# Kernel tuning notes

Hardware: AMD Instinct MI355X
Metric: run time of the kernel (lower is better)

The kernel has to match this reference:

```python
import jax, jax.numpy as jnp
import numpy as np

N_FRAMES = 100000
HIDDEN = 512
N_QUERIES = 256
N_EVENTS = 2048
TOPK = 8
FRAME_RATE = 5.0
EPS = 1e-12


def setup_inputs() -> dict:
    key = jax.random.key(0)
    k1, k2, k3, k4 = jax.random.split(key, 4)
    video_feats = jax.random.normal(k1, (1, N_FRAMES, HIDDEN), dtype=jnp.float32)
    query_feats = jax.random.normal(k2, (N_QUERIES, HIDDEN), dtype=jnp.float32)
    video_events = jnp.sort(
        jax.random.randint(k3, (N_FRAMES,), 0, N_EVENTS, dtype=jnp.int32))
    W_reg = jax.random.normal(k4, (HIDDEN, 2), dtype=jnp.float32) * 0.02
    b_reg = jnp.zeros((2,), dtype=jnp.float32)
    return {"video_feats": video_feats, "query_feats": query_feats,
            "video_events": video_events, "W_reg": W_reg, "b_reg": b_reg}


def reference(video_feats, query_feats, video_events, W_reg, b_reg):
    vf = video_feats[0]                                   # [N, D]
    n = vf.shape[0]
    # --- per-event masked-mean pooling (segment mean) ---
    sums = jax.ops.segment_sum(vf, video_events, num_segments=N_EVENTS)          # [E, D]
    counts = jax.ops.segment_sum(jnp.ones((n,), vf.dtype), video_events,
                                 num_segments=N_EVENTS)                          # [E]
    event_avg = sums / jnp.maximum(counts, 1.0)[:, None]                         # [E, D]
    # --- event timestamps: first/last frame index per event / frame_rate ---
    idx = jnp.arange(n, dtype=jnp.int32)
    start = jax.ops.segment_min(idx, video_events, num_segments=N_EVENTS)
    end = jax.ops.segment_max(idx, video_events, num_segments=N_EVENTS)
    # empty events get int extremes; zero them out (they have zero features anyway)
    nonempty = counts > 0
    start = jnp.where(nonempty, start, 0)
    end = jnp.where(nonempty, end, 0)
    event_ts = jnp.stack([start, end], axis=-1).astype(jnp.float32) / FRAME_RATE  # [E, 2]
    # --- cosine similarity query x event ---
    qn = query_feats / jnp.maximum(
        jnp.linalg.norm(query_feats, axis=-1, keepdims=True), EPS)
    en = event_avg / jnp.maximum(
        jnp.linalg.norm(event_avg, axis=-1, keepdims=True), EPS)
    sim = qn @ en.T                                       # [Q, E]
    # --- per-query top-k event selection ---
    _, top_idx = jax.lax.top_k(sim, TOPK)                 # [Q, K]
    sel_ts = event_ts[top_idx]                            # [Q, K, 2]
    sel_dur = sel_ts[..., 1] - sel_ts[..., 0]             # [Q, K]
    sel_feat = event_avg[top_idx]                         # [Q, K, D]
    interact = sel_feat * query_feats[:, None, :]         # [Q, K, D]
    bbox_bias = jnp.tanh(jnp.einsum('qkd,dt->qkt', interact, W_reg) + b_reg)  # [Q, K, 2]
    pred_timestamps = sel_ts + bbox_bias * sel_dur[..., None]
    return pred_timestamps
```

## Files before the change

### kernel.cpp

```cpp
#include <hip/hip_runtime.h>
#include <hip/hip_bf16.h>
#include <math.h>

#define N_FRAMES 100000
#define HIDDEN 512
#define N_QUERIES 256
#define N_EVENTS 2048
#define TOPK 8
#define FRAME_RATE 5.0f
#define EPSN 1e-12f


__global__ void init_k(int* __restrict__ start, int* __restrict__ end) {
    int e = blockIdx.x * blockDim.x + threadIdx.x;
    if (e < N_EVENTS) { start[e] = -1; end[e] = -1; }
}

__global__ void bounds_k(const int* __restrict__ ev, int* __restrict__ start,
                         int* __restrict__ end) {
    int i = blockIdx.x * blockDim.x + threadIdx.x;
    if (i >= N_FRAMES) return;
    int e = ev[i];
    if (i == 0 || ev[i - 1] != e) start[e] = i;
    if (i == N_FRAMES - 1 || ev[i + 1] != e) end[e] = i;
}

__global__ void pool_k(const float* __restrict__ vf, const int* __restrict__ start,
                       const int* __restrict__ end, float* __restrict__ avg,
                       float* __restrict__ inv_en, float* __restrict__ ts) {
    int e = blockIdx.x;
    int s = start[e], t = end[e];
    int tid = threadIdx.x;
    int half = tid >> 7;
    int l = tid & 127;
    float4 acc = make_float4(0.f, 0.f, 0.f, 0.f);
    if (s >= 0) {
        const float4* p = (const float4*)vf + (size_t)(s + half) * 128 + l;
        int f = s + half;
        for (; f + 2 <= t; f += 4, p += 512) {
            float4 v0 = p[0];
            float4 v1 = p[256];
            acc.x += v0.x + v1.x; acc.y += v0.y + v1.y;
            acc.z += v0.z + v1.z; acc.w += v0.w + v1.w;
        }
        if (f <= t) {
            float4 v0 = *p;
            acc.x += v0.x; acc.y += v0.y; acc.z += v0.z; acc.w += v0.w;
        }
    }
    __shared__ float4 buf[128];
    __shared__ float ssbuf[2];
    if (half) buf[l] = acc;
    __syncthreads();
    if (!half) {
        float4 o = buf[l];
        acc.x += o.x; acc.y += o.y; acc.z += o.z; acc.w += o.w;
        if (s >= 0) {
            float cnt = (float)(t - s + 1);
            acc.x = acc.x / cnt; acc.y = acc.y / cnt;
            acc.z = acc.z / cnt; acc.w = acc.w / cnt;
        }
        *((float4*)avg + (size_t)e * 128 + l) = acc;
        float ss = acc.x * acc.x + acc.y * acc.y + acc.z * acc.z + acc.w * acc.w;
        #pragma unroll
        for (int off = 32; off; off >>= 1) ss += __shfl_xor(ss, off);
        if ((tid & 63) == 0) ssbuf[tid >> 6] = ss;
    }
    __syncthreads();
    if (tid == 0) {
        float ss = ssbuf[0] + ssbuf[1];
        inv_en[e] = (s >= 0) ? 1.0f / fmaxf(sqrtf(ss), EPSN) : 0.0f;
        ts[e * 2 + 0] = (s >= 0) ? (float)s / FRAME_RATE : 0.0f;
        ts[e * 2 + 1] = (s >= 0) ? (float)t / FRAME_RATE : 0.0f;
    }
}

__global__ void qnorm_k(const float* __restrict__ qf, float* __restrict__ inv_qn) {
    int q = blockIdx.x;
    int lane = threadIdx.x;
    const float* row = qf + (size_t)q * HIDDEN;
    float ss = 0.f;
    #pragma unroll
    for (int i = 0; i < 8; ++i) { float v = row[lane + 64 * i]; ss += v * v; }
    #pragma unroll
    for (int off = 32; off; off >>= 1) ss += __shfl_xor(ss, off);
    if (lane == 0) inv_qn[q] = 1.0f / fmaxf(sqrtf(ss), EPSN);
}

#define BQ 64
#define BE 32
#define DC 128
#define DCP 132

__global__ void sim_k(const float* __restrict__ qf, const float* __restrict__ avg,
                      const float* __restrict__ inv_qn, const float* __restrict__ inv_en,
                      float* __restrict__ sim) {
    __shared__ float qs[BQ][DCP];
    __shared__ float es[BE][DCP];
    int tid = threadIdx.x;
    int qbase = blockIdx.y * BQ;
    int ebase = blockIdx.x * BE;
    int e0 = tid & 15;
    int q0 = tid >> 4;
    float acc[4][2] = {{0.f, 0.f}, {0.f, 0.f}, {0.f, 0.f}, {0.f, 0.f}};
    for (int dc = 0; dc < HIDDEN; dc += DC) {
        __syncthreads();
        #pragma unroll
        for (int r = 0; r < 8; ++r) {
            int ldx = tid + 256 * r;
            int row = ldx >> 5, c4 = ldx & 31;
            float4 v = *(const float4*)(qf + (size_t)(qbase + row) * HIDDEN + dc + c4 * 4);
            *(float4*)&qs[row][c4 * 4] = v;
        }
        #pragma unroll
        for (int r = 0; r < 4; ++r) {
            int ldx = tid + 256 * r;
            int row = ldx >> 5, c4 = ldx & 31;
            float4 v = *(const float4*)(avg + (size_t)(ebase + row) * HIDDEN + dc + c4 * 4);
            *(float4*)&es[row][c4 * 4] = v;
        }
        __syncthreads();
        #pragma unroll 4
        for (int d = 0; d < DC; d += 4) {
            float4 ev0 = *(const float4*)&es[e0][d];
            float4 ev1 = *(const float4*)&es[e0 + 16][d];
            #pragma unroll
            for (int i = 0; i < 4; ++i) {
                float4 qv = *(const float4*)&qs[q0 + 16 * i][d];
                acc[i][0] += qv.x * ev0.x + qv.y * ev0.y + qv.z * ev0.z + qv.w * ev0.w;
                acc[i][1] += qv.x * ev1.x + qv.y * ev1.y + qv.z * ev1.z + qv.w * ev1.w;
            }
        }
    }
    float iq[4];
    #pragma unroll
    for (int i = 0; i < 4; ++i) iq[i] = inv_qn[qbase + q0 + 16 * i];
    float ie0 = inv_en[ebase + e0];
    float ie1 = inv_en[ebase + e0 + 16];
    #pragma unroll
    for (int i = 0; i < 4; ++i) {
        size_t rowoff = (size_t)(qbase + q0 + 16 * i) * N_EVENTS + ebase;
        sim[rowoff + e0] = acc[i][0] * iq[i] * ie0;
        sim[rowoff + e0 + 16] = acc[i][1] * iq[i] * ie1;
    }
}

__global__ void topk_k(const float* __restrict__ sim, int* __restrict__ top_idx) {
    int q = blockIdx.x;
    int lane = threadIdx.x;
    const float* row = sim + (size_t)q * N_EVENTS;
    float v[32];
    #pragma unroll
    for (int i = 0; i < 32; ++i) v[i] = row[lane + 64 * i];
    int chosen[TOPK];
    #pragma unroll
    for (int k = 0; k < TOPK; ++k) {
        float best = -INFINITY;
        int bidx = 0x7fffffff;
        #pragma unroll
        for (int i = 0; i < 32; ++i) {
            int idx = lane + 64 * i;
            bool dup = false;
            #pragma unroll
            for (int j = 0; j < TOPK; ++j) dup = dup || ((j < k) && (chosen[j] == idx));
            if (!dup && v[i] > best) { best = v[i]; bidx = idx; }
        }
        #pragma unroll
        for (int off = 32; off; off >>= 1) {
            float ov = __shfl_xor(best, off);
            int oi = __shfl_xor(bidx, off);
            if (ov > best || (ov == best && oi < bidx)) { best = ov; bidx = oi; }
        }
        chosen[k] = bidx;
        if (lane == 0) top_idx[q * TOPK + k] = bidx;
    }
}

__global__ void final_k(const float* __restrict__ avg, const float* __restrict__ qf,
                        const float* __restrict__ ts, const int* __restrict__ top_idx,
                        const float* __restrict__ W, const float* __restrict__ b,
                        float* __restrict__ out) {
    int blk = blockIdx.x;
    int q = blk >> 3;
    int lane = threadIdx.x;
    int e = top_idx[blk];
    const float* frow = avg + (size_t)e * HIDDEN;
    const float* qrow = qf + (size_t)q * HIDDEN;
    float a0 = 0.f, a1 = 0.f;
    #pragma unroll
    for (int i = 0; i < 8; ++i) {
        int d = lane + 64 * i;
        float f = frow[d] * qrow[d];
        a0 += f * W[d * 2 + 0];
        a1 += f * W[d * 2 + 1];
    }
    #pragma unroll
    for (int off = 32; off; off >>= 1) {
        a0 += __shfl_xor(a0, off);
        a1 += __shfl_xor(a1, off);
    }
    if (lane == 0) {
        float b0 = tanhf(a0 + b[0]);
        float b1 = tanhf(a1 + b[1]);
        float t0 = ts[e * 2 + 0], t1 = ts[e * 2 + 1];
        float dur = t1 - t0;
        out[blk * 2 + 0] = t0 + b0 * dur;
        out[blk * 2 + 1] = t1 + b1 * dur;
    }
}

extern "C" void kernel_launch(void* const* d_in, const int* in_sizes, int n_in,
                              void* d_out, int out_size, void* d_ws, size_t ws_size,
                              hipStream_t stream) {
    const float* vf = (const float*)d_in[0];
    const float* qf = (const float*)d_in[1];
    const int* ev = (const int*)d_in[2];
    const float* W = (const float*)d_in[3];
    const float* b = (const float*)d_in[4];
    float* out = (float*)d_out;

    char* ws = (char*)d_ws;
    float* avg    = (float*)(ws + 0);
    float* ts     = (float*)(ws + 4194304);
    float* inv_en = (float*)(ws + 4210688);
    float* inv_qn = (float*)(ws + 4218880);
    int*   start  = (int*)  (ws + 4219904);
    int*   endp   = (int*)  (ws + 4228096);
    float* sim    = (float*)(ws + 4236288);
    int*   tidx   = (int*)  (ws + 6333440);

    init_k<<<(N_EVENTS + 255) / 256, 256, 0, stream>>>(start, endp);
    bounds_k<<<(N_FRAMES + 255) / 256, 256, 0, stream>>>(ev, start, endp);
    pool_k<<<N_EVENTS, 256, 0, stream>>>(vf, start, endp, avg, inv_en, ts);
    qnorm_k<<<N_QUERIES, 64, 0, stream>>>(qf, inv_qn);
    dim3 sgrid(N_EVENTS / BE, N_QUERIES / BQ);
    sim_k<<<sgrid, 256, 0, stream>>>(qf, avg, inv_qn, inv_en, sim);
    topk_k<<<N_QUERIES, 64, 0, stream>>>(sim, tidx);
    final_k<<<N_QUERIES * TOPK, 64, 0, stream>>>(avg, qf, ts, tidx, W, b, out);
}
```

Baseline: 335.0 us.

## Fuse init with query norm, merge topk with regressor, enlarge sim tiles

Merges the event-bounds init and the query-norm kernels into one launch, and fuses top-k selection with the bbox regressor so the top indices stay in registers and each query's weights and features are loaded once. The similarity kernel moves to 128 threads, each computing a 4x4 output tile instead of 4x2. Top-k now reads the sim row as float4. The net effect is two fewer launches and less global traffic, at the cost of lower parallelism in the final stage and in sim_k.

New measurement: 352.4 us. +5.2%, slower.

```diff
diff --git a/kernel.cpp b/kernel.cpp
--- a/kernel.cpp
+++ b/kernel.cpp
@@ -11,9 +11,22 @@
 #define EPSN 1e-12f
 
 
-__global__ void init_k(int* __restrict__ start, int* __restrict__ end) {
-    int e = blockIdx.x * blockDim.x + threadIdx.x;
-    if (e < N_EVENTS) { start[e] = -1; end[e] = -1; }
+__global__ void initq_k(const float* __restrict__ qf, float* __restrict__ inv_qn,
+                        int* __restrict__ start, int* __restrict__ end) {
+    int blk = blockIdx.x;
+    int lane = threadIdx.x;
+    if (blk < N_QUERIES) {
+        const float* row = qf + (size_t)blk * HIDDEN;
+        float ss = 0.f;
+        #pragma unroll
+        for (int i = 0; i < 8; ++i) { float v = row[lane + 64 * i]; ss += v * v; }
+        #pragma unroll
+        for (int off = 32; off; off >>= 1) ss += __shfl_xor(ss, off);
+        if (lane == 0) inv_qn[blk] = 1.0f / fmaxf(sqrtf(ss), EPSN);
+    } else {
+        int e = (blk - N_QUERIES) * 64 + lane;
+        start[e] = -1; end[e] = -1;
+    }
 }
 
 __global__ void bounds_k(const int* __restrict__ ev, int* __restrict__ start,
@@ -57,8 +70,7 @@
         acc.x += o.x; acc.y += o.y; acc.z += o.z; acc.w += o.w;
         if (s >= 0) {
             float cnt = (float)(t - s + 1);
-            acc.x = acc.x / cnt; acc.y = acc.y / cnt;
-            acc.z = acc.z / cnt; acc.w = acc.w / cnt;
+            acc.x /= cnt; acc.y /= cnt; acc.z /= cnt; acc.w /= cnt;
         }
         *((float4*)avg + (size_t)e * 128 + l) = acc;
         float ss = acc.x * acc.x + acc.y * acc.y + acc.z * acc.z + acc.w * acc.w;
@@ -73,18 +85,6 @@
         ts[e * 2 + 0] = (s >= 0) ? (float)s / FRAME_RATE : 0.0f;
         ts[e * 2 + 1] = (s >= 0) ? (float)t / FRAME_RATE : 0.0f;
     }
-}
-
-__global__ void qnorm_k(const float* __restrict__ qf, float* __restrict__ inv_qn) {
-    int q = blockIdx.x;
-    int lane = threadIdx.x;
-    const float* row = qf + (size_t)q * HIDDEN;
-    float ss = 0.f;
-    #pragma unroll
-    for (int i = 0; i < 8; ++i) { float v = row[lane + 64 * i]; ss += v * v; }
-    #pragma unroll
-    for (int off = 32; off; off >>= 1) ss += __shfl_xor(ss, off);
-    if (lane == 0) inv_qn[q] = 1.0f / fmaxf(sqrtf(ss), EPSN);
 }
 
 #define BQ 64
@@ -100,70 +100,85 @@
     int tid = threadIdx.x;
     int qbase = blockIdx.y * BQ;
     int ebase = blockIdx.x * BE;
-    int e0 = tid & 15;
-    int q0 = tid >> 4;
-    float acc[4][2] = {{0.f, 0.f}, {0.f, 0.f}, {0.f, 0.f}, {0.f, 0.f}};
+    int q0 = tid >> 3;
+    int e0 = tid & 7;
+    float acc[4][4] = {{0.f,0.f,0.f,0.f},{0.f,0.f,0.f,0.f},
+                       {0.f,0.f,0.f,0.f},{0.f,0.f,0.f,0.f}};
     for (int dc = 0; dc < HIDDEN; dc += DC) {
         __syncthreads();
         #pragma unroll
+        for (int r = 0; r < 16; ++r) {
+            int ldx = tid + 128 * r;
+            int row = ldx >> 5, c4 = ldx & 31;
+            *(float4*)&qs[row][c4 * 4] =
+                *(const float4*)(qf + (size_t)(qbase + row) * HIDDEN + dc + c4 * 4);
+        }
+        #pragma unroll
         for (int r = 0; r < 8; ++r) {
-            int ldx = tid + 256 * r;
+            int ldx = tid + 128 * r;
             int row = ldx >> 5, c4 = ldx & 31;
-            float4 v = *(const float4*)(qf + (size_t)(qbase + row) * HIDDEN + dc + c4 * 4);
-            *(float4*)&qs[row][c4 * 4] = v;
-        }
-        #pragma unroll
-        for (int r = 0; r < 4; ++r) {
-            int ldx = tid + 256 * r;
-            int row = ldx >> 5, c4 = ldx & 31;
-            float4 v = *(const float4*)(avg + (size_t)(ebase + row) * HIDDEN + dc + c4 * 4);
-            *(float4*)&es[row][c4 * 4] = v;
+            *(float4*)&es[row][c4 * 4] =
+                *(const float4*)(avg + (size_t)(ebase + row) * HIDDEN + dc + c4 * 4);
         }
         __syncthreads();
-        #pragma unroll 4
+        #pragma unroll 2
         for (int d = 0; d < DC; d += 4) {
             float4 ev0 = *(const float4*)&es[e0][d];
-            float4 ev1 = *(const float4*)&es[e0 + 16][d];
+            float4 ev1 = *(const float4*)&es[e0 + 8][d];
+            float4 ev2 = *(const float4*)&es[e0 + 16][d];
+            float4 ev3 = *(const float4*)&es[e0 + 24][d];
             #pragma unroll
             for (int i = 0; i < 4; ++i) {
                 float4 qv = *(const float4*)&qs[q0 + 16 * i][d];
                 acc[i][0] += qv.x * ev0.x + qv.y * ev0.y + qv.z * ev0.z + qv.w * ev0.w;
                 acc[i][1] += qv.x * ev1.x + qv.y * ev1.y + qv.z * ev1.z + qv.w * ev1.w;
+                acc[i][2] += qv.x * ev2.x + qv.y * ev2.y + qv.z * ev2.z + qv.w * ev2.w;
+                acc[i][3] += qv.x * ev3.x + qv.y * ev3.y + qv.z * ev3.z + qv.w * ev3.w;
             }
         }
     }
-    float iq[4];
+    float iq[4], ie[4];
     #pragma unroll
     for (int i = 0; i < 4; ++i) iq[i] = inv_qn[qbase + q0 + 16 * i];
-    float ie0 = inv_en[ebase + e0];
-    float ie1 = inv_en[ebase + e0 + 16];
+    #pragma unroll
+    for (int j = 0; j < 4; ++j) ie[j] = inv_en[ebase + e0 + 8 * j];
     #pragma unroll
     for (int i = 0; i < 4; ++i) {
         size_t rowoff = (size_t)(qbase + q0 + 16 * i) * N_EVENTS + ebase;
-        sim[rowoff + e0] = acc[i][0] * iq[i] * ie0;
-        sim[rowoff + e0 + 16] = acc[i][1] * iq[i] * ie1;
-    }
-}
-
-__global__ void topk_k(const float* __restrict__ sim, int* __restrict__ top_idx) {
+        #pragma unroll
+        for (int j = 0; j < 4; ++j)
+            sim[rowoff + e0 + 8 * j] = acc[i][j] * iq[i] * ie[j];
+    }
+}
+
+__global__ void topk_final_k(const float* __restrict__ sim, const float* __restrict__ ts,
+                             const float* __restrict__ avg, const float* __restrict__ qf,
+                             const float* __restrict__ W, const float* __restrict__ b,
+                             float* __restrict__ out) {
     int q = blockIdx.x;
     int lane = threadIdx.x;
-    const float* row = sim + (size_t)q * N_EVENTS;
-    float v[32];
-    #pragma unroll
-    for (int i = 0; i < 32; ++i) v[i] = row[lane + 64 * i];
+    const float4* row4 = (const float4*)(sim + (size_t)q * N_EVENTS);
+    float4 v4[8];
+    #pragma unroll
+    for (int g = 0; g < 8; ++g) v4[g] = row4[lane + 64 * g];
     int chosen[TOPK];
     #pragma unroll
     for (int k = 0; k < TOPK; ++k) {
         float best = -INFINITY;
         int bidx = 0x7fffffff;
         #pragma unroll
-        for (int i = 0; i < 32; ++i) {
-            int idx = lane + 64 * i;
-            bool dup = false;
+        for (int g = 0; g < 8; ++g) {
             #pragma unroll
-            for (int j = 0; j < TOPK; ++j) dup = dup || ((j < k) && (chosen[j] == idx));
-            if (!dup && v[i] > best) { best = v[i]; bidx = idx; }
+            for (int j = 0; j < 4; ++j) {
+                int idx = 4 * lane + 256 * g + j;
+                float val = (j == 0) ? v4[g].x : (j == 1) ? v4[g].y
+                          : (j == 2) ? v4[g].z : v4[g].w;
+                bool dup = false;
+                #pragma unroll
+                for (int m = 0; m < TOPK; ++m)
+                    dup = dup || ((m < k) && (chosen[m] == idx));
+                if (!dup && val > best) { best = val; bidx = idx; }
+            }
         }
         #pragma unroll
         for (int off = 32; off; off >>= 1) {
@@ -172,40 +187,37 @@
             if (ov > best || (ov == best && oi < bidx)) { best = ov; bidx = oi; }
         }
         chosen[k] = bidx;
-        if (lane == 0) top_idx[q * TOPK + k] = bidx;
-    }
-}
-
-__global__ void final_k(const float* __restrict__ avg, const float* __restrict__ qf,
-                        const float* __restrict__ ts, const int* __restrict__ top_idx,
-                        const float* __restrict__ W, const float* __restrict__ b,
-                        float* __restrict__ out) {
-    int blk = blockIdx.x;
-    int q = blk >> 3;
-    int lane = threadIdx.x;
-    int e = top_idx[blk];
-    const float* frow = avg + (size_t)e * HIDDEN;
+    }
     const float* qrow = qf + (size_t)q * HIDDEN;
-    float a0 = 0.f, a1 = 0.f;
-    #pragma unroll
-    for (int i = 0; i < 8; ++i) {
-        int d = lane + 64 * i;
-        float f = frow[d] * qrow[d];
-        a0 += f * W[d * 2 + 0];
-        a1 += f * W[d * 2 + 1];
-    }
-    #pragma unroll
-    for (int off = 32; off; off >>= 1) {
-        a0 += __shfl_xor(a0, off);
-        a1 += __shfl_xor(a1, off);
-    }
-    if (lane == 0) {
-        float b0 = tanhf(a0 + b[0]);
-        float b1 = tanhf(a1 + b[1]);
-        float t0 = ts[e * 2 + 0], t1 = ts[e * 2 + 1];
-        float dur = t1 - t0;
-        out[blk * 2 + 0] = t0 + b0 * dur;
-        out[blk * 2 + 1] = t1 + b1 * dur;
+    float qreg[8];
+    float2 wreg[8];
+    #pragma unroll
+    for (int i = 0; i < 8; ++i) qreg[i] = qrow[lane + 64 * i];
+    #pragma unroll
+    for (int i = 0; i < 8; ++i) wreg[i] = ((const float2*)W)[lane + 64 * i];
+    float b0s = b[0], b1s = b[1];
+    #pragma unroll
+    for (int k = 0; k < TOPK; ++k) {
+        int e = chosen[k];
+        const float* frow = avg + (size_t)e * HIDDEN;
+        float a0 = 0.f, a1 = 0.f;
+        #pragma unroll
+        for (int i = 0; i < 8; ++i) {
+            float f = frow[lane + 64 * i] * qreg[i];
+            a0 += f * wreg[i].x;
+            a1 += f * wreg[i].y;
+        }
+        #pragma unroll
+        for (int off = 32; off; off >>= 1) {
+            a0 += __shfl_xor(a0, off);
+            a1 += __shfl_xor(a1, off);
+        }
+        if (lane == 0) {
+            float t0 = ts[e * 2 + 0], t1 = ts[e * 2 + 1];
+            float dur = t1 - t0;
+            out[(q * TOPK + k) * 2 + 0] = t0 + tanhf(a0 + b0s) * dur;
+            out[(q * TOPK + k) * 2 + 1] = t1 + tanhf(a1 + b1s) * dur;
+        }
     }
 }
 
@@ -227,14 +239,11 @@
     int*   start  = (int*)  (ws + 4219904);
     int*   endp   = (int*)  (ws + 4228096);
     float* sim    = (float*)(ws + 4236288);
-    int*   tidx   = (int*)  (ws + 6333440);
-
-    init_k<<<(N_EVENTS + 255) / 256, 256, 0, stream>>>(start, endp);
+
+    initq_k<<<N_QUERIES + N_EVENTS / 64, 64, 0, stream>>>(qf, inv_qn, start, endp);
     bounds_k<<<(N_FRAMES + 255) / 256, 256, 0, stream>>>(ev, start, endp);
     pool_k<<<N_EVENTS, 256, 0, stream>>>(vf, start, endp, avg, inv_en, ts);
-    qnorm_k<<<N_QUERIES, 64, 0, stream>>>(qf, inv_qn);
     dim3 sgrid(N_EVENTS / BE, N_QUERIES / BQ);
-    sim_k<<<sgrid, 256, 0, stream>>>(qf, avg, inv_qn, inv_en, sim);
-    topk_k<<<N_QUERIES, 64, 0, stream>>>(sim, tidx);
-    final_k<<<N_QUERIES * TOPK, 64, 0, stream>>>(avg, qf, ts, tidx, W, b, out);
-}
+    sim_k<<<sgrid, 128, 0, stream>>>(qf, avg, inv_qn, inv_en, sim);
+    topk_final_k<<<N_QUERIES, 64, 0, stream>>>(sim, ts, avg, qf, W, b, out);
+}
```
